# Optimization experiments

Hardware: AMD Instinct MI355X
Metric: run time of the kernel (lower is better)

## Reference

```python
import jax, jax.numpy as jnp
import numpy as np

B, L, C, N, D, FF, L2 = 1, 2400, 1536, 12, 128, 8960, 512
F_, H_, W_ = 2, 30, 40  # grid: L = F*H*W
EPS = 1e-6


def _rope_table(max_len=1024, d=D):
    # Wan rope_params: three bands of sizes d-4*(d//6), 2*(d//6), 2*(d//6)
    parts = [d - 4 * (d // 6), 2 * (d // 6), 2 * (d // 6)]
    pos = np.arange(max_len, dtype=np.float32)
    cs, ss = [], []
    for dp in parts:
        inv = 1.0 / (10000.0 ** (np.arange(0, dp, 2, dtype=np.float32) / dp))
        ang = np.outer(pos, inv)
        cs.append(np.cos(ang)); ss.append(np.sin(ang))
    return np.stack([np.concatenate(cs, 1), np.concatenate(ss, 1)], -1)  # [1024, d//2, 2]


def setup_inputs() -> dict:
    key = jax.random.key(0)
    ks = iter(jax.random.split(key, 48))
    def rn(shape, s=0.02):
        return jax.random.normal(next(ks), shape, dtype=jnp.float32) * s
    inp = dict(
        x=jax.random.normal(next(ks), (B, L, C), dtype=jnp.float32),
        e=rn((B, 1, 6, C), 0.5),
        context=jax.random.normal(next(ks), (B, L2, C), dtype=jnp.float32),
        freqs=jnp.asarray(_rope_table()),
        seq_lens=jnp.full((B,), L, dtype=jnp.int32),
        context_lens=jnp.full((B,), L2, dtype=jnp.int32),
        grid_sizes=jnp.array([[F_, H_, W_]], dtype=jnp.int32),
        modulation=rn((1, 6, C), 0.5),
    )
    for p in ('sa', 'ca'):
        for w in ('q', 'k', 'v', 'o'):
            inp[f'{p}_{w}_w'] = rn((C, C))
            inp[f'{p}_{w}_b'] = rn((C,))
        inp[f'{p}_nq_w'] = jnp.ones((C,), jnp.float32)
        inp[f'{p}_nk_w'] = jnp.ones((C,), jnp.float32)
    inp['ffn_w1'] = rn((C, FF)); inp['ffn_b1'] = rn((FF,))
    inp['ffn_w2'] = rn((FF, C)); inp['ffn_b2'] = rn((C,))
    return inp


def _rms_norm(x, w):
    v = jnp.mean(jnp.square(x), axis=-1, keepdims=True)
    return x * jax.lax.rsqrt(v + EPS) * w


def _layer_norm(x):
    m = jnp.mean(x, axis=-1, keepdims=True)
    v = jnp.mean(jnp.square(x - m), axis=-1, keepdims=True)
    return (x - m) * jax.lax.rsqrt(v + EPS)


def _apply_rope(x, freqs):
    # x: [B,S,N,D]; freqs: [1024, D//2, 2] (cos, sin). Wan default rope.
    c = D // 2
    p0, p1 = c - 2 * (c // 3), c // 3
    ft = jnp.broadcast_to(freqs[:F_, None, None, :p0], (F_, H_, W_, p0, 2))
    fh = jnp.broadcast_to(freqs[None, :H_, None, p0:p0 + p1], (F_, H_, W_, p1, 2))
    fw = jnp.broadcast_to(freqs[None, None, :W_, p0 + p1:], (F_, H_, W_, c - p0 - p1, 2))
    fr = jnp.concatenate([ft, fh, fw], axis=3).reshape(L, c, 2)
    cos = fr[..., 0][None, :, None, :]  # [1,S,1,c]
    sin = fr[..., 1][None, :, None, :]
    xp = x.reshape(B, x.shape[1], N, c, 2)  # interleaved (real, imag) pairs
    xr, xi = xp[..., 0], xp[..., 1]
    out = jnp.stack([xr * cos - xi * sin, xr * sin + xi * cos], axis=-1)
    return out.reshape(x.shape)


def _attention(q, k, v, k_len):
    # q:[B,Sq,N,D] k,v:[B,Sk,N,D]; dense softmax attention with k_lens mask
    scale = 1.0 / jnp.sqrt(jnp.float32(D))
    scores = jnp.einsum('bqnd,bknd->bnqk', q, k) * scale
    mask = jnp.arange(k.shape[1])[None, None, None, :] < k_len[:, None, None, None]
    scores = jnp.where(mask, scores, -jnp.inf)
    p = jax.nn.softmax(scores, axis=-1)
    return jnp.einsum('bnqk,bknd->bqnd', p, v)


def reference(x, e, context, freqs, seq_lens, context_lens, grid_sizes, modulation,
              sa_q_w, sa_q_b, sa_k_w, sa_k_b, sa_v_w, sa_v_b, sa_o_w, sa_o_b, sa_nq_w, sa_nk_w,
              ca_q_w, ca_q_b, ca_k_w, ca_k_b, ca_v_w, ca_v_b, ca_o_w, ca_o_b, ca_nq_w, ca_nk_w,
              ffn_w1, ffn_b1, ffn_w2, ffn_b2):
    # e: [B,1,6,C] (L1=1, broadcast over L == repeat_e); modulation: [1,6,C]
    em = modulation[None] + e  # [B,1,6,C]
    e0, e1, e2, e3, e4, e5 = (em[:, :, i] for i in range(6))  # each [B,1,C]
    # --- self attention with modulation ---
    h = e0 + _layer_norm(x) * (1.0 + e1)
    q = _rms_norm(h @ sa_q_w + sa_q_b, sa_nq_w).reshape(B, L, N, D)
    k = _rms_norm(h @ sa_k_w + sa_k_b, sa_nk_w).reshape(B, L, N, D)
    v = (h @ sa_v_w + sa_v_b).reshape(B, L, N, D)
    q = _apply_rope(q, freqs)
    k = _apply_rope(k, freqs)
    y = _attention(q, k, v, seq_lens).reshape(B, L, C)
    y = y @ sa_o_w + sa_o_b
    x = x + y * e2
    # --- cross attention (norm3 = Identity, cross_attn_norm=False) ---
    q = _rms_norm(x @ ca_q_w + ca_q_b, ca_nq_w).reshape(B, L, N, D)
    k = _rms_norm(context @ ca_k_w + ca_k_b, ca_nk_w).reshape(B, L2, N, D)
    v = (context @ ca_v_w + ca_v_b).reshape(B, L2, N, D)
    y = _attention(q, k, v, context_lens).reshape(B, L, C)
    x = x + (y @ ca_o_w + ca_o_b)
    # --- FFN with modulation ---
    h = e3 + _layer_norm(x) * (1.0 + e4)
    y = jax.nn.gelu(h @ ffn_w1 + ffn_b1, approximate=True) @ ffn_w2 + ffn_b2
    x = x + y * e5
    return x
```

## Files before the change

kernel.cpp:

```cpp
#include <hip/hip_runtime.h>
#include <cstddef>
#include <cstdint>

#define C_DIM   1536
#define L_SEQ   2400
#define L_CTX   512
#define N_HEADS 12
#define D_HEAD  128
#define FF_DIM  8960
#define F_GRID  2
#define H_GRID  30
#define W_GRID  40
#define EPS_F   1e-6f

#define ROPE_P0 22
#define ROPE_P1 43

typedef __attribute__((ext_vector_type(8))) short short8;
typedef __attribute__((ext_vector_type(4))) float f32x4;

__device__ inline unsigned short f2bf(float f) {
    union { float f; unsigned int u; } v; v.f = f;
    unsigned int r = v.u + 0x7FFF + ((v.u >> 16) & 1);
    return (unsigned short)(r >> 16);
}

#define GL2LDS(gp, lp) \
    __builtin_amdgcn_global_load_lds((const __attribute__((address_space(1))) void*)(gp), \
                                     (__attribute__((address_space(3))) void*)(lp), 16, 0, 0)

#define VMCNT6() asm volatile("s_waitcnt vmcnt(6)" ::: "memory")
#define VMCNT0() asm volatile("s_waitcnt vmcnt(0)" ::: "memory")
#define LGKM0()  asm volatile("s_waitcnt lgkmcnt(0)" ::: "memory")
#define BAR()    __builtin_amdgcn_s_barrier()


__global__ __launch_bounds__(256) void k_embed(const float* __restrict__ mod,
                                               const float* __restrict__ e,
                                               float* __restrict__ ev, int n) {
    int i = blockIdx.x * 256 + threadIdx.x;
    if (i < n) ev[i] = mod[i] + e[i];
}

__global__ __launch_bounds__(256) void k_catbias(float* __restrict__ dst,
                                                 const float* __restrict__ b0,
                                                 const float* __restrict__ b1,
                                                 const float* __restrict__ b2,
                                                 int ne, int n) {
    int i = blockIdx.x * 256 + threadIdx.x;
    if (i >= n) return;
    const float* s = (i < ne) ? b0 : (i < 2 * ne) ? b1 : b2;
    dst[i] = s[i % ne];
}

__global__ __launch_bounds__(256) void k_initbias(float* __restrict__ C,
                                                  const float* __restrict__ bias,
                                                  int n, int N) {
    int i4 = (blockIdx.x * 256 + threadIdx.x) * 4;
    if (i4 >= n) return;
    int col = i4 % N;
    *(float4*)(C + i4) = *(const float4*)(bias + col);
}

__global__ __launch_bounds__(256) void k_resid2(const float* __restrict__ a,
                                                const float* __restrict__ b,
                                                const float* __restrict__ ev, int ei,
                                                float* __restrict__ out,
                                                unsigned short* __restrict__ outb, int n) {
    int i = (blockIdx.x * 256 + threadIdx.x) * 2;
    if (i >= n) return;
    int c = i % C_DIM;
    float s0 = 1.f, s1 = 1.f;
    if (ei >= 0) {
        s0 = ev[ei * C_DIM + c];
        s1 = ev[ei * C_DIM + c + 1];
    }
    float2 av = *(const float2*)(a + i);
    float2 bv = *(const float2*)(b + i);
    float o0 = av.x + bv.x * s0;
    float o1 = av.y + bv.y * s1;
    *(float2*)(out + i) = make_float2(o0, o1);
    if (outb) {
        unsigned int pk = (unsigned int)f2bf(o0) | ((unsigned int)f2bf(o1) << 16);
        *(unsigned int*)(outb + i) = pk;
    }
}

__global__ __launch_bounds__(256) void k_tobf(const float* __restrict__ X,
                                              unsigned short* __restrict__ Y, int n) {
    int i = (blockIdx.x * 256 + threadIdx.x) * 2;
    if (i >= n) return;
    float2 v = *(const float2*)(X + i);
    unsigned int pk = (unsigned int)f2bf(v.x) | ((unsigned int)f2bf(v.y) << 16);
    *(unsigned int*)(Y + i) = pk;
}

__global__ __launch_bounds__(256) void k_lnmod_bf16(const float* __restrict__ X,
                                                    const float* __restrict__ ev,
                                                    int i0, int i1,
                                                    unsigned short* __restrict__ H) {
    __shared__ float rs[256];
    __shared__ float rs2[256];
    int row = blockIdx.x, tid = threadIdx.x;
    const float* xr = X + (size_t)row * C_DIM;
    float2 vals[3];
    float s = 0.f, s2 = 0.f;
#pragma unroll
    for (int i = 0; i < 3; ++i) {
        float2 v = *(const float2*)(xr + 2 * (tid + 256 * i));
        vals[i] = v;
        s += v.x + v.y; s2 += v.x * v.x + v.y * v.y;
    }
    rs[tid] = s; rs2[tid] = s2;
    __syncthreads();
    for (int st = 128; st > 0; st >>= 1) {
        if (tid < st) { rs[tid] += rs[tid + st]; rs2[tid] += rs2[tid + st]; }
        __syncthreads();
    }
    float mean = rs[0] * (1.0f / C_DIM);
    float var  = rs2[0] * (1.0f / C_DIM) - mean * mean;
    float rinv = rsqrtf(var + EPS_F);
    const float* E0 = ev + (size_t)i0 * C_DIM;
    const float* E1 = ev + (size_t)i1 * C_DIM;
    unsigned short* hr = H + (size_t)row * C_DIM;
#pragma unroll
    for (int i = 0; i < 3; ++i) {
        int c = 2 * (tid + 256 * i);
        float o0 = E0[c]     + (vals[i].x - mean) * rinv * (1.0f + E1[c]);
        float o1 = E0[c + 1] + (vals[i].y - mean) * rinv * (1.0f + E1[c + 1]);
        unsigned int pk = (unsigned int)f2bf(o0) | ((unsigned int)f2bf(o1) << 16);
        *(unsigned int*)(hr + c) = pk;
    }
}

__global__ __launch_bounds__(256) void k_rms_rope_bf16(const float* __restrict__ X,
                                                       const float* __restrict__ w,
                                                       const float* __restrict__ freqs,
                                                       int do_rope, float outscale,
                                                       unsigned short* __restrict__ Y,
                                                       int ldx) {
    __shared__ float rs[256];
    int row = blockIdx.x, tid = threadIdx.x;
    const float* xr = X + (size_t)row * ldx;
    float2 vals[3];
    float ss = 0.f;
#pragma unroll
    for (int i = 0; i < 3; ++i) {
        int p = tid + 256 * i;
        float2 v = *(const float2*)(xr + 2 * p);
        vals[i] = v;
        ss += v.x * v.x + v.y * v.y;
    }
    rs[tid] = ss;
    __syncthreads();
    for (int st = 128; st > 0; st >>= 1) {
        if (tid < st) rs[tid] += rs[tid + st];
        __syncthreads();
    }
    float rinv = rsqrtf(rs[0] * (1.0f / C_DIM) + EPS_F);
    int f = row / (H_GRID * W_GRID);
    int rem = row % (H_GRID * W_GRID);
    int hh = rem / W_GRID, ww = rem % W_GRID;
    unsigned short* yr = Y + (size_t)row * C_DIM;
#pragma unroll
    for (int i = 0; i < 3; ++i) {
        int p = tid + 256 * i;
        int c = 2 * p;
        float a = vals[i].x * rinv * w[c];
        float b = vals[i].y * rinv * w[c + 1];
        if (do_rope) {
            int j = p & 63;
            int idx = (j < ROPE_P0) ? f : (j < ROPE_P1) ? hh : ww;
            float cv = freqs[(idx * 64 + j) * 2 + 0];
            float sv = freqs[(idx * 64 + j) * 2 + 1];
            float na = a * cv - b * sv;
            float nb = a * sv + b * cv;
            a = na; b = nb;
        }
        a *= outscale; b *= outscale;
        unsigned int pk = (unsigned int)f2bf(a) | ((unsigned int)f2bf(b) << 16);
        *(unsigned int*)(yr + c) = pk;
    }
}

__global__ __launch_bounds__(256) void k_wt(const float* __restrict__ W,
                                            unsigned short* __restrict__ WT,
                                            int K, int N) {
    __shared__ float tile[32][33];
    int k0 = blockIdx.x * 32, n0 = blockIdx.y * 32;
    int t = threadIdx.x;
    int r = t >> 3, c4 = (t & 7) * 4;
    float4 v = *(const float4*)(W + (size_t)(k0 + r) * N + n0 + c4);
    tile[r][c4 + 0] = v.x; tile[r][c4 + 1] = v.y;
    tile[r][c4 + 2] = v.z; tile[r][c4 + 3] = v.w;
    __syncthreads();
    int n = t >> 3, k4 = (t & 7) * 4;
    uint2 o;
    o.x = (unsigned int)f2bf(tile[k4 + 0][n]) | ((unsigned int)f2bf(tile[k4 + 1][n]) << 16);
    o.y = (unsigned int)f2bf(tile[k4 + 2][n]) | ((unsigned int)f2bf(tile[k4 + 3][n]) << 16);
    *(uint2*)(WT + (size_t)(n0 + n) * K + k0 + k4) = o;
}

__global__ __launch_bounds__(256) void k_vt(const float* __restrict__ V,
                                            unsigned short* __restrict__ Vt, int Lk, int ldv) {
    __shared__ float tile[32][33];
    int k0 = blockIdx.x * 32, h = blockIdx.y, d0 = blockIdx.z * 32;
    int t = threadIdx.x;
    int k = t >> 3, d4 = (t & 7) * 4;
    float4 v = *(const float4*)(V + (size_t)(k0 + k) * ldv + h * D_HEAD + d0 + d4);
    tile[k][d4 + 0] = v.x; tile[k][d4 + 1] = v.y;
    tile[k][d4 + 2] = v.z; tile[k][d4 + 3] = v.w;
    __syncthreads();
    int d = t >> 3, k4 = (t & 7) * 4;
    uint2 o;
    o.x = (unsigned int)f2bf(tile[k4 + 0][d]) | ((unsigned int)f2bf(tile[k4 + 1][d]) << 16);
    o.y = (unsigned int)f2bf(tile[k4 + 2][d]) | ((unsigned int)f2bf(tile[k4 + 3][d]) << 16);
    *(uint2*)(Vt + (size_t)(h * D_HEAD + d0 + d) * Lk + k0 + k4) = o;
}

__global__ __launch_bounds__(256) void k_attn_mfma(const unsigned short* __restrict__ Qb,
                                                   const unsigned short* __restrict__ Kb,
                                                   const unsigned short* __restrict__ Vt,
                                                   unsigned short* __restrict__ O,
                                                   int Lq, int Lk) {
    __shared__ __align__(16) unsigned short Ks[32][136];
    __shared__ __align__(16) unsigned short Vs[128][40];
    __shared__ __align__(16) unsigned short Ps[4][16][40];
    const int tid = threadIdx.x;
    const int w = tid >> 6, lane = tid & 63;
    const int ln = lane & 15, lq = lane >> 4;
    const int h = blockIdx.y;
    const int q0 = blockIdx.x * 64 + w * 16;
    int qrow = q0 + ln; if (qrow >= Lq) qrow = Lq - 1;
    short8 qf[4];
#pragma unroll
    for (int c = 0; c < 4; ++c)
        qf[c] = *(const short8*)(Qb + (size_t)qrow * C_DIM + h * D_HEAD + c * 32 + lq * 8);
    f32x4 oacc[8];
#pragma unroll
    for (int t = 0; t < 8; ++t) oacc[t] = (f32x4){0.f, 0.f, 0.f, 0.f};
    float m_run[4] = {-3e38f, -3e38f, -3e38f, -3e38f};
    float l_run[4] = {0.f, 0.f, 0.f, 0.f};
    const float LOG2E = 1.4426950408889634f;

    for (int kb = 0; kb < Lk; kb += 32) {
        __syncthreads();
#pragma unroll
        for (int i = 0; i < 2; ++i) {
            int id = tid + i * 256;
            int r = id >> 4, c = id & 15;
            *(uint4*)&Ks[r][c * 8] =
                *(const uint4*)(Kb + (size_t)(kb + r) * C_DIM + h * D_HEAD + c * 8);
            int d = id >> 2, c2 = id & 3;
            *(uint4*)&Vs[d][c2 * 8] =
                *(const uint4*)(Vt + (size_t)(h * D_HEAD + d) * Lk + kb + c2 * 8);
        }
        __syncthreads();
        f32x4 c0 = (f32x4){0.f, 0.f, 0.f, 0.f};
        f32x4 c1 = (f32x4){0.f, 0.f, 0.f, 0.f};
#pragma unroll
        for (int c = 0; c < 4; ++c) {
            short8 b0 = *(const short8*)&Ks[ln][c * 32 + lq * 8];
            short8 b1 = *(const short8*)&Ks[16 + ln][c * 32 + lq * 8];
            c0 = __builtin_amdgcn_mfma_f32_16x16x32_bf16(qf[c], b0, c0, 0, 0, 0);
            c1 = __builtin_amdgcn_mfma_f32_16x16x32_bf16(qf[c], b1, c1, 0, 0, 0);
        }
        float alpha[4];
#pragma unroll
        for (int r = 0; r < 4; ++r) {
            float mx = fmaxf(c0[r], c1[r]);
            mx = fmaxf(mx, __shfl_xor(mx, 1));
            mx = fmaxf(mx, __shfl_xor(mx, 2));
            mx = fmaxf(mx, __shfl_xor(mx, 4));
            mx = fmaxf(mx, __shfl_xor(mx, 8));
            float mn = fmaxf(m_run[r], mx);
            alpha[r] = exp2f((m_run[r] - mn) * LOG2E);
            float p0 = exp2f((c0[r] - mn) * LOG2E);
            float p1 = exp2f((c1[r] - mn) * LOG2E);
            float s = p0 + p1;
            s += __shfl_xor(s, 1);
            s += __shfl_xor(s, 2);
            s += __shfl_xor(s, 4);
            s += __shfl_xor(s, 8);
            l_run[r] = l_run[r] * alpha[r] + s;
            m_run[r] = mn;
            Ps[w][lq * 4 + r][ln] = f2bf(p0);
            Ps[w][lq * 4 + r][16 + ln] = f2bf(p1);
        }
#pragma unroll
        for (int t = 0; t < 8; ++t)
#pragma unroll
            for (int r = 0; r < 4; ++r) oacc[t][r] *= alpha[r];
        short8 pa = *(const short8*)&Ps[w][ln][lq * 8];
#pragma unroll
        for (int t = 0; t < 8; ++t) {
            short8 bv = *(const short8*)&Vs[t * 16 + ln][lq * 8];
            oacc[t] = __builtin_amdgcn_mfma_f32_16x16x32_bf16(pa, bv, oacc[t], 0, 0, 0);
        }
    }
    float linv[4];
#pragma unroll
    for (int r = 0; r < 4; ++r) linv[r] = 1.0f / l_run[r];
#pragma unroll
    for (int t = 0; t < 8; ++t)
#pragma unroll
        for (int r = 0; r < 4; ++r) {
            int row = q0 + lq * 4 + r;
            if (row < Lq)
                O[(size_t)row * C_DIM + h * D_HEAD + t * 16 + ln] = f2bf(oacc[t][r] * linv[r]);
        }
}

__global__ __launch_bounds__(256) void k_gemm_bf16(const unsigned short* __restrict__ A,
                                                   const unsigned short* __restrict__ BT,
                                                   const float* __restrict__ bias,
                                                   float* __restrict__ Cf,
                                                   unsigned short* __restrict__ Cb,
                                                   int M, int N, int K, int Kc,
                                                   int gelu, int atomic) {
    __shared__ __align__(16) unsigned short As[128 * 32];
    __shared__ __align__(16) unsigned short Bs[128 * 32];
    const int tid = threadIdx.x;
    const int lane = tid & 63;
    const int w = tid >> 6;
    const int ln = lane & 15, lq = lane >> 4;
    const int wm = w >> 1, wn = w & 1;
    const int bm = blockIdx.y * 128, bn = blockIdx.x * 128;
    const int kb0 = blockIdx.z * Kc;

    int r0 = tid >> 2, c0 = (tid & 3) * 8;
    int ar0 = bm + r0;      if (ar0 >= M) ar0 = M - 1;
    int ar1 = bm + r0 + 64; if (ar1 >= M) ar1 = M - 1;
    const unsigned short* Ag0 = A + (size_t)ar0 * K + c0;
    const unsigned short* Ag1 = A + (size_t)ar1 * K + c0;
    const unsigned short* Bg0 = BT + (size_t)(bn + r0) * K + c0;
    const unsigned short* Bg1 = BT + (size_t)(bn + r0 + 64) * K + c0;
    unsigned short* Al0 = As + tid * 8;
    unsigned short* Al1 = As + 2048 + tid * 8;
    unsigned short* Bl0 = Bs + tid * 8;
    unsigned short* Bl1 = Bs + 2048 + tid * 8;

    f32x4 acc[4][4];
#pragma unroll
    for (int i = 0; i < 4; ++i)
#pragma unroll
        for (int j = 0; j < 4; ++j) acc[i][j] = (f32x4){0.f, 0.f, 0.f, 0.f};

    for (int kb = kb0; kb < kb0 + Kc; kb += 32) {
        __syncthreads();
        GL2LDS(Ag0 + kb, Al0);
        GL2LDS(Ag1 + kb, Al1);
        GL2LDS(Bg0 + kb, Bl0);
        GL2LDS(Bg1 + kb, Bl1);
        __syncthreads();
        short8 af[4], bf[4];
#pragma unroll
        for (int mi = 0; mi < 4; ++mi)
            af[mi] = *(const short8*)&As[(wm * 64 + mi * 16 + ln) * 32 + lq * 8];
#pragma unroll
        for (int ni = 0; ni < 4; ++ni)
            bf[ni] = *(const short8*)&Bs[(wn * 64 + ni * 16 + ln) * 32 + lq * 8];
#pragma unroll
        for (int mi = 0; mi < 4; ++mi)
#pragma unroll
            for (int ni = 0; ni < 4; ++ni)
                acc[mi][ni] = __builtin_amdgcn_mfma_f32_16x16x32_bf16(af[mi], bf[ni],
                                                                      acc[mi][ni], 0, 0, 0);
    }

#pragma unroll
    for (int ni = 0; ni < 4; ++ni) {
        int col = bn + wn * 64 + ni * 16 + ln;
        float bv = atomic ? 0.f : bias[col];
#pragma unroll
        for (int mi = 0; mi < 4; ++mi) {
#pragma unroll
            for (int r = 0; r < 4; ++r) {
                int row = bm + wm * 64 + mi * 16 + lq * 4 + r;
                if (row >= M) continue;
                if (atomic) {
                    atomicAdd(Cf + (size_t)row * N + col, acc[mi][ni][r]);
                } else if (gelu) {
                    float v = acc[mi][ni][r] + bv;
                    float u = 0.7978845608028654f * (v + 0.044715f * v * v * v);
                    float ex = __expf(2.f * u);
                    float t = 1.f - 2.f / (ex + 1.f);
                    Cb[(size_t)row * N + col] = f2bf(0.5f * v * (1.f + t));
                } else {
                    Cf[(size_t)row * N + col] = acc[mi][ni][r] + bv;
                }
            }
        }
    }
}

__global__ __launch_bounds__(512, 2) void k_gemm256(const unsigned short* __restrict__ A,
                                                    const unsigned short* __restrict__ BT,
                                                    const float* __restrict__ bias,
                                                    float* __restrict__ Cf,
                                                    unsigned short* __restrict__ Cb,
                                                    int M, int N, int K, int Kc,
                                                    int gelu, int atomic) {
    __shared__ __align__(16) unsigned short lds[2][2][2][128 * 64];
    const int tid = threadIdx.x;
    const int wid = tid >> 6, lane = tid & 63;
    const int ln = lane & 15, lq = lane >> 4;
    const int wm = wid >> 2, wn = wid & 3;
    const int bm = blockIdx.y * 256, bn = blockIdx.x * 256;
    const int kb0 = blockIdx.z * Kc;
    const int NT = Kc >> 6;
    const int NI = (NT + 1) >> 1;

    const int rr = tid >> 3;
    const int cc = (((tid & 7) ^ (rr & 7)) * 8);
    const unsigned short* aP[4];
    const unsigned short* bP[4];
#pragma unroll
    for (int g = 0; g < 4; ++g) {
        int ar = bm + g * 64 + rr; if (ar >= M) ar = M - 1;
        aP[g] = A + (size_t)ar * K + cc + kb0;
        bP[g] = BT + (size_t)(bn + g * 64 + rr) * K + cc + kb0;
    }

    f32x4 acc[8][4];
#pragma unroll
    for (int i = 0; i < 8; ++i)
#pragma unroll
        for (int j = 0; j < 4; ++j) acc[i][j] = (f32x4){0.f, 0.f, 0.f, 0.f};

    short8 af[4][2], bf0[2][2], bf1[2][2];

    const unsigned short* A0 = &lds[0][0][wm][0];
    const unsigned short* A1 = &lds[1][0][wm][0];
    const unsigned short* B0 = &lds[0][1][wn >> 1][0];
    const unsigned short* B1 = &lds[1][1][wn >> 1][0];

    auto stgA = [&](unsigned short* dst, int h, int kt) {
        GL2LDS(aP[h * 2 + 0] + (size_t)kt * 64, dst + tid * 8);
        GL2LDS(aP[h * 2 + 1] + (size_t)kt * 64, dst + 4096 + tid * 8);
    };
    auto stgB = [&](unsigned short* dst, int h, int kt) {
        GL2LDS(bP[h * 2 + 0] + (size_t)kt * 64, dst + tid * 8);
        GL2LDS(bP[h * 2 + 1] + (size_t)kt * 64, dst + 4096 + tid * 8);
    };
    auto rdA = [&](const unsigned short* Ab_, int mh) {
#pragma unroll
        for (int m4 = 0; m4 < 4; ++m4) {
            const int row = mh * 64 + m4 * 16 + ln;
#pragma unroll
            for (int ks = 0; ks < 2; ++ks) {
                const int sl = (ks * 4 + lq) ^ (ln & 7);
                af[m4][ks] = *(const short8*)&Ab_[row * 64 + sl * 8];
            }
        }
    };
    auto rdB = [&](const unsigned short* Bb_, int nh, short8 (&bfX)[2][2]) {
#pragma unroll
        for (int n2 = 0; n2 < 2; ++n2) {
            const int row = (wn & 1) * 64 + (nh * 2 + n2) * 16 + ln;
#pragma unroll
            for (int ks = 0; ks < 2; ++ks) {
                const int sl = (ks * 4 + lq) ^ (ln & 7);
                bfX[n2][ks] = *(const short8*)&Bb_[row * 64 + sl * 8];
            }
        }
    };
    auto mm = [&](int mh, int nh, short8 (&bfX)[2][2]) {
        __builtin_amdgcn_s_setprio(1);
#pragma unroll
        for (int m4 = 0; m4 < 4; ++m4)
#pragma unroll
            for (int n2 = 0; n2 < 2; ++n2)
#pragma unroll
                for (int ks = 0; ks < 2; ++ks)
                    acc[mh * 4 + m4][nh * 2 + n2] = __builtin_amdgcn_mfma_f32_16x16x32_bf16(
                        af[m4][ks], bfX[n2][ks], acc[mh * 4 + m4][nh * 2 + n2], 0, 0, 0);
        __builtin_amdgcn_s_setprio(0);
    };

    stgB(&lds[0][1][0][0], 0, 0); stgB(&lds[0][1][1][0], 1, 0);
    stgA(&lds[0][0][0][0], 0, 0);
    stgA(&lds[0][0][1][0], 1, 0);
    stgB(&lds[1][1][0][0], 0, 1);
    stgA(&lds[1][0][0][0], 0, 1); stgB(&lds[1][1][1][0], 1, 1);
    VMCNT6(); BAR();

    for (int k0 = 0; k0 < NI; ++k0) {
        const int a = 2 * k0, bT = a + 1;
        const bool last = (k0 == NI - 1);
        const bool hasB = (bT < NT);
        rdA(A0, 0); rdB(B0, 0, bf0);
        if (hasB) stgA(&lds[1][0][1][0], 1, bT);
        BAR(); LGKM0();
        mm(0, 0, bf0);
        BAR();
        rdB(B0, 1, bf1);
        BAR(); LGKM0();
        mm(0, 1, bf1);
        BAR();
        rdA(A0, 1);
        if (a + 2 < NT) { stgB(&lds[0][1][0][0], 0, a + 2); stgB(&lds[0][1][1][0], 1, a + 2); }
        BAR(); LGKM0();
        mm(1, 1, bf1);
        BAR();
        if (a + 2 < NT) stgA(&lds[0][0][0][0], 0, a + 2);
        BAR();
        mm(1, 0, bf0);
        if (!hasB) { BAR(); break; }
        if (last) { VMCNT0(); } else { VMCNT6(); }
        BAR();
        rdA(A1, 0); rdB(B1, 0, bf0);
        if (a + 2 < NT) stgA(&lds[0][0][1][0], 1, a + 2);
        BAR(); LGKM0();
        mm(0, 0, bf0);
        BAR();
        rdB(B1, 1, bf1);
        BAR(); LGKM0();
        mm(0, 1, bf1);
        BAR();
        rdA(A1, 1);
        if (bT + 2 < NT) stgB(&lds[1][1][0][0], 0, bT + 2);
        BAR(); LGKM0();
        mm(1, 1, bf1);
        BAR();
        if (bT + 2 < NT) { stgA(&lds[1][0][0][0], 0, bT + 2); stgB(&lds[1][1][1][0], 1, bT + 2); }
        BAR();
        mm(1, 0, bf0);
        if (k0 >= NI - 2) { VMCNT0(); } else { VMCNT6(); }
        BAR();
    }

#pragma unroll
    for (int ni = 0; ni < 4; ++ni) {
        int col = bn + wn * 64 + ni * 16 + ln;
        float bv = atomic ? 0.f : bias[col];
#pragma unroll
        for (int mi = 0; mi < 8; ++mi) {
#pragma unroll
            for (int r = 0; r < 4; ++r) {
                int row = bm + wm * 128 + mi * 16 + lq * 4 + r;
                if (row >= M) continue;
                if (atomic) {
                    atomicAdd(Cf + (size_t)row * N + col, acc[mi][ni][r]);
                } else if (gelu) {
                    float v = acc[mi][ni][r] + bv;
                    float u = 0.7978845608028654f * (v + 0.044715f * v * v * v);
                    float ex = __expf(2.f * u);
                    float t = 1.f - 2.f / (ex + 1.f);
                    Cb[(size_t)row * N + col] = f2bf(0.5f * v * (1.f + t));
                } else {
                    Cf[(size_t)row * N + col] = acc[mi][ni][r] + bv;
                }
            }
        }
    }
}

extern "C" void kernel_launch(void* const* d_in, const int* in_sizes, int n_in,
                              void* d_out, int out_size, void* d_ws, size_t ws_size,
                              hipStream_t stream) {
    const float* x          = (const float*)d_in[0];
    const float* e          = (const float*)d_in[1];
    const float* context    = (const float*)d_in[2];
    const float* freqs      = (const float*)d_in[3];
    const float* modulation = (const float*)d_in[7];
    const float* sa_q_w = (const float*)d_in[8];
    const float* sa_q_b = (const float*)d_in[9];
    const float* sa_k_w = (const float*)d_in[10];
    const float* sa_k_b = (const float*)d_in[11];
    const float* sa_v_w = (const float*)d_in[12];
    const float* sa_v_b = (const float*)d_in[13];
    const float* sa_o_w = (const float*)d_in[14];
    const float* sa_o_b = (const float*)d_in[15];
    const float* sa_nq  = (const float*)d_in[16];
    const float* sa_nk  = (const float*)d_in[17];
    const float* ca_q_w = (const float*)d_in[18];
    const float* ca_q_b = (const float*)d_in[19];
    const float* ca_k_w = (const float*)d_in[20];
    const float* ca_k_b = (const float*)d_in[21];
    const float* ca_v_w = (const float*)d_in[22];
    const float* ca_v_b = (const float*)d_in[23];
    const float* ca_o_w = (const float*)d_in[24];
    const float* ca_o_b = (const float*)d_in[25];
    const float* ca_nq  = (const float*)d_in[26];
    const float* ca_nk  = (const float*)d_in[27];
    const float* ffn_w1 = (const float*)d_in[28];
    const float* ffn_b1 = (const float*)d_in[29];
    const float* ffn_w2 = (const float*)d_in[30];
    const float* ffn_b2 = (const float*)d_in[31];

    const size_t LC = (size_t)L_SEQ * C_DIM;
    const size_t WMAX = (size_t)C_DIM * FF_DIM;
    char* p = (char*)d_ws;
    float* ev   = (float*)p;            p += 6 * C_DIM * sizeof(float);
    float* Bcat = (float*)p;            p += 3 * C_DIM * sizeof(float);
    float* Xcur = (float*)p;            p += LC * sizeof(float);
    float* Ebuf = (float*)p;            p += LC * sizeof(float);
    float* QKV  = (float*)p;            p += 3 * LC * sizeof(float);
    unsigned short* Ab = (unsigned short*)p;  p += LC * sizeof(short);
    unsigned short* Xb = (unsigned short*)p;  p += LC * sizeof(short);
    unsigned short* Qb = (unsigned short*)p;  p += LC * sizeof(short);
    unsigned short* Kb = (unsigned short*)p;  p += LC * sizeof(short);
    unsigned short* Vt = (unsigned short*)p;  p += LC * sizeof(short);
    unsigned short* Ob = (unsigned short*)p;  p += LC * sizeof(short);
    unsigned short* W0 = (unsigned short*)p;  p += WMAX * sizeof(short);
    unsigned short* W1 = (unsigned short*)p;  p += WMAX * sizeof(short);
    unsigned short* Fb = (unsigned short*)QKV;
    float* Pq    = QKV;
    float* ctxKV = QKV + LC;

    const int nLC = (int)LC;
    const float SCALE = 0.08838834764831845f;
    dim3 blk(256);
    dim3 blk512(512);
    dim3 g_qkv_256(4608 / 256, 10, 1);
    dim3 g_proj_s4(C_DIM / 128, 19, 4);
    dim3 g_ctxkv_s4(3072 / 128, L_CTX / 128, 4);
    dim3 g_ff1_256(FF_DIM / 256, 10, 1);
    dim3 g_ff2_256(C_DIM / 256, 10, 4);
    dim3 g_attn((L_SEQ + 63) / 64, N_HEADS);
    dim3 g_vt_s(L_SEQ / 32, N_HEADS, 4);
    dim3 g_vt_c(L_CTX / 32, N_HEADS, 4);
    dim3 g_wt_cc(C_DIM / 32, C_DIM / 32);
    dim3 g_wt_w1(C_DIM / 32, FF_DIM / 32);
    dim3 g_wt_w2(FF_DIM / 32, C_DIM / 32);
    dim3 g_half(nLC / 512);
    dim3 g_init_cc(nLC / 1024);
    dim3 g_init_kv(L_CTX * 3072 / 1024);

    k_embed<<<dim3((6 * C_DIM + 255) / 256), blk, 0, stream>>>(modulation, e, ev, 6 * C_DIM);

    k_catbias<<<dim3((3 * C_DIM + 255) / 256), blk, 0, stream>>>(Bcat, sa_q_b, sa_k_b, sa_v_b,
                                                                 C_DIM, 3 * C_DIM);
    k_wt<<<g_wt_cc, blk, 0, stream>>>(sa_q_w, W0, C_DIM, C_DIM);
    k_wt<<<g_wt_cc, blk, 0, stream>>>(sa_k_w, W0 + (size_t)C_DIM * C_DIM, C_DIM, C_DIM);
    k_wt<<<g_wt_cc, blk, 0, stream>>>(sa_v_w, W0 + (size_t)2 * C_DIM * C_DIM, C_DIM, C_DIM);
    k_lnmod_bf16<<<dim3(L_SEQ), blk, 0, stream>>>(x, ev, 0, 1, Ab);
    k_gemm256<<<g_qkv_256, blk512, 0, stream>>>(Ab, W0, Bcat, QKV, nullptr,
                                                L_SEQ, 4608, C_DIM, C_DIM, 0, 0);
    k_wt<<<g_wt_cc, blk, 0, stream>>>(sa_o_w, W1, C_DIM, C_DIM);
    k_rms_rope_bf16<<<dim3(L_SEQ), blk, 0, stream>>>(QKV, sa_nq, freqs, 1, SCALE, Qb, 4608);
    k_rms_rope_bf16<<<dim3(L_SEQ), blk, 0, stream>>>(QKV + C_DIM, sa_nk, freqs, 1, 1.0f, Kb, 4608);
    k_vt<<<g_vt_s, blk, 0, stream>>>(QKV + 2 * C_DIM, Vt, L_SEQ, 4608);
    k_attn_mfma<<<g_attn, blk, 0, stream>>>(Qb, Kb, Vt, Ob, L_SEQ, L_SEQ);
    k_initbias<<<g_init_cc, blk, 0, stream>>>(Ebuf, sa_o_b, nLC, C_DIM);
    k_gemm_bf16<<<g_proj_s4, blk, 0, stream>>>(Ob, W1, nullptr, Ebuf, nullptr,
                                               L_SEQ, C_DIM, C_DIM, 384, 0, 1);
    k_resid2<<<g_half, blk, 0, stream>>>(x, Ebuf, ev, 2, Xcur, Xb, nLC);

    k_wt<<<g_wt_cc, blk, 0, stream>>>(ca_q_w, W0, C_DIM, C_DIM);
    k_wt<<<g_wt_cc, blk, 0, stream>>>(ca_k_w, W1, C_DIM, C_DIM);
    k_wt<<<g_wt_cc, blk, 0, stream>>>(ca_v_w, W1 + (size_t)C_DIM * C_DIM, C_DIM, C_DIM);
    k_tobf<<<dim3(L_CTX * C_DIM / 512), blk, 0, stream>>>(context, Ab, L_CTX * C_DIM);
    k_catbias<<<dim3((2 * C_DIM + 255) / 256), blk, 0, stream>>>(Bcat, ca_k_b, ca_v_b, nullptr,
                                                                 C_DIM, 2 * C_DIM);
    k_initbias<<<g_init_cc, blk, 0, stream>>>(Pq, ca_q_b, nLC, C_DIM);
    k_gemm_bf16<<<g_proj_s4, blk, 0, stream>>>(Xb, W0, nullptr, Pq, nullptr,
                                               L_SEQ, C_DIM, C_DIM, 384, 0, 1);
    k_initbias<<<g_init_kv, blk, 0, stream>>>(ctxKV, Bcat, L_CTX * 3072, 3072);
    k_gemm_bf16<<<g_ctxkv_s4, blk, 0, stream>>>(Ab, W1, nullptr, ctxKV, nullptr,
                                                L_CTX, 3072, C_DIM, 384, 0, 1);
    k_rms_rope_bf16<<<dim3(L_SEQ), blk, 0, stream>>>(Pq, ca_nq, freqs, 0, SCALE, Qb, C_DIM);
    k_rms_rope_bf16<<<dim3(L_CTX), blk, 0, stream>>>(ctxKV, ca_nk, freqs, 0, 1.0f, Kb, 3072);
    k_vt<<<g_vt_c, blk, 0, stream>>>(ctxKV + C_DIM, Vt, L_CTX, 3072);
    k_attn_mfma<<<g_attn, blk, 0, stream>>>(Qb, Kb, Vt, Ob, L_SEQ, L_CTX);
    k_wt<<<g_wt_cc, blk, 0, stream>>>(ca_o_w, W0, C_DIM, C_DIM);
    k_initbias<<<g_init_cc, blk, 0, stream>>>(Ebuf, ca_o_b, nLC, C_DIM);
    k_gemm_bf16<<<g_proj_s4, blk, 0, stream>>>(Ob, W0, nullptr, Ebuf, nullptr,
                                               L_SEQ, C_DIM, C_DIM, 384, 0, 1);
    k_resid2<<<g_half, blk, 0, stream>>>(Xcur, Ebuf, (const float*)nullptr, -1, Xcur, nullptr, nLC);

    k_wt<<<g_wt_w1, blk, 0, stream>>>(ffn_w1, W1, C_DIM, FF_DIM);
    k_lnmod_bf16<<<dim3(L_SEQ), blk, 0, stream>>>(Xcur, ev, 3, 4, Ab);
    k_gemm256<<<g_ff1_256, blk512, 0, stream>>>(Ab, W1, ffn_b1, nullptr, Fb,
                                                L_SEQ, FF_DIM, C_DIM, C_DIM, 1, 0);
    k_wt<<<g_wt_w2, blk, 0, stream>>>(ffn_w2, W0, FF_DIM, C_DIM);
    k_initbias<<<g_init_cc, blk, 0, stream>>>(Ebuf, ffn_b2, nLC, C_DIM);
    k_gemm256<<<g_ff2_256, blk512, 0, stream>>>(Fb, W0, nullptr, Ebuf, nullptr,
                                                L_SEQ, C_DIM, FF_DIM, 2240, 0, 1);
    k_resid2<<<g_half, blk, 0, stream>>>(Xcur, Ebuf, ev, 5, (float*)d_out, nullptr, nLC);
}
```

Before: 1.098 ms.

## Widen attention key tiles with swizzled async loads and lazy rescale; route projections to 256-tile GEMM

The attention kernel now processes 64 keys per iteration instead of 32. K and V tiles are loaded straight into XOR-swizzled shared memory with global-to-LDS copies, which avoids bank conflicts and register staging. It also skips the rescale of the output accumulator unless the running max grows by more than a threshold (lazy rescaling). Separately, the 128-tile projection GEMM is removed and all projection and context K/V GEMMs use the 256-tile kernel with split-K. This cuts barriers and per-tile overhead in attention, but the threshold-based rescale could cause overflow issues and edge handling for partial tiles grows more complex.

Measured after the change: 1.042 ms. 5.1% less time.

```diff
diff --git a/kernel.cpp b/kernel.cpp
--- a/kernel.cpp
+++ b/kernel.cpp
@@ -223,9 +223,9 @@
                                                    const unsigned short* __restrict__ Vt,
                                                    unsigned short* __restrict__ O,
                                                    int Lq, int Lk) {
-    __shared__ __align__(16) unsigned short Ks[32][136];
-    __shared__ __align__(16) unsigned short Vs[128][40];
-    __shared__ __align__(16) unsigned short Ps[4][16][40];
+    __shared__ __align__(16) unsigned short Ks[64 * 128];
+    __shared__ __align__(16) unsigned short Vs[128 * 64];
+    __shared__ __align__(16) unsigned short Ps[4][16][68];
     const int tid = threadIdx.x;
     const int w = tid >> 6, lane = tid & 63;
     const int ln = lane & 15, lq = lane >> 4;
@@ -236,66 +236,113 @@
 #pragma unroll
     for (int c = 0; c < 4; ++c)
         qf[c] = *(const short8*)(Qb + (size_t)qrow * C_DIM + h * D_HEAD + c * 32 + lq * 8);
+
+    const int r0k = tid >> 4, sk = tid & 15;
+    const int kxor = r0k & 7;
+    const int kcol = h * D_HEAD + (sk ^ kxor) * 8;
+    int rowK[4];
+    unsigned short* dK[4];
+#pragma unroll
+    for (int j = 0; j < 4; ++j) {
+        rowK[j] = r0k + 16 * j;
+        dK[j] = (unsigned short*)Ks + ((size_t)tid + 256 * j) * 8;
+    }
+    const int d0v = tid >> 3, sv = tid & 7;
+    const int vxor = d0v & 7;
+    const int vslot = (sv ^ vxor) * 8;
+    int dRow[4];
+    unsigned short* dV[4];
+#pragma unroll
+    for (int j = 0; j < 4; ++j) {
+        dRow[j] = h * D_HEAD + d0v + 32 * j;
+        dV[j] = (unsigned short*)Vs + ((size_t)tid + 256 * j) * 8;
+    }
+
     f32x4 oacc[8];
 #pragma unroll
     for (int t = 0; t < 8; ++t) oacc[t] = (f32x4){0.f, 0.f, 0.f, 0.f};
     float m_run[4] = {-3e38f, -3e38f, -3e38f, -3e38f};
     float l_run[4] = {0.f, 0.f, 0.f, 0.f};
     const float LOG2E = 1.4426950408889634f;
-
-    for (int kb = 0; kb < Lk; kb += 32) {
+    const int lx = ln & 7;
+
+    for (int kb = 0; kb < Lk; kb += 64) {
+        const bool gv2 = (kb + 32) < Lk;
         __syncthreads();
 #pragma unroll
-        for (int i = 0; i < 2; ++i) {
-            int id = tid + i * 256;
-            int r = id >> 4, c = id & 15;
-            *(uint4*)&Ks[r][c * 8] =
-                *(const uint4*)(Kb + (size_t)(kb + r) * C_DIM + h * D_HEAD + c * 8);
-            int d = id >> 2, c2 = id & 3;
-            *(uint4*)&Vs[d][c2 * 8] =
-                *(const uint4*)(Vt + (size_t)(h * D_HEAD + d) * Lk + kb + c2 * 8);
+        for (int j = 0; j < 4; ++j) {
+            int kr = kb + rowK[j]; if (kr >= Lk) kr = Lk - 1;
+            GL2LDS(Kb + (size_t)kr * C_DIM + kcol, dK[j]);
+            int vc = kb + vslot; if (vc + 8 > Lk) vc = Lk - 8;
+            GL2LDS(Vt + (size_t)dRow[j] * Lk + vc, dV[j]);
         }
         __syncthreads();
-        f32x4 c0 = (f32x4){0.f, 0.f, 0.f, 0.f};
-        f32x4 c1 = (f32x4){0.f, 0.f, 0.f, 0.f};
+
+        f32x4 c0 = (f32x4){0.f,0.f,0.f,0.f}, c1 = c0, c2 = c0, c3 = c0;
 #pragma unroll
         for (int c = 0; c < 4; ++c) {
-            short8 b0 = *(const short8*)&Ks[ln][c * 32 + lq * 8];
-            short8 b1 = *(const short8*)&Ks[16 + ln][c * 32 + lq * 8];
+            const int slt = ((c * 4 + lq) ^ lx) * 8;
+            short8 b0 = *(const short8*)&Ks[(size_t)(ln) * 128 + slt];
+            short8 b1 = *(const short8*)&Ks[(size_t)(16 + ln) * 128 + slt];
             c0 = __builtin_amdgcn_mfma_f32_16x16x32_bf16(qf[c], b0, c0, 0, 0, 0);
             c1 = __builtin_amdgcn_mfma_f32_16x16x32_bf16(qf[c], b1, c1, 0, 0, 0);
-        }
-        float alpha[4];
+            if (gv2) {
+                short8 b2 = *(const short8*)&Ks[(size_t)(32 + ln) * 128 + slt];
+                short8 b3 = *(const short8*)&Ks[(size_t)(48 + ln) * 128 + slt];
+                c2 = __builtin_amdgcn_mfma_f32_16x16x32_bf16(qf[c], b2, c2, 0, 0, 0);
+                c3 = __builtin_amdgcn_mfma_f32_16x16x32_bf16(qf[c], b3, c3, 0, 0, 0);
+            }
+        }
+
 #pragma unroll
         for (int r = 0; r < 4; ++r) {
             float mx = fmaxf(c0[r], c1[r]);
+            if (gv2) mx = fmaxf(mx, fmaxf(c2[r], c3[r]));
             mx = fmaxf(mx, __shfl_xor(mx, 1));
             mx = fmaxf(mx, __shfl_xor(mx, 2));
             mx = fmaxf(mx, __shfl_xor(mx, 4));
             mx = fmaxf(mx, __shfl_xor(mx, 8));
-            float mn = fmaxf(m_run[r], mx);
-            alpha[r] = exp2f((m_run[r] - mn) * LOG2E);
+            float mn = m_run[r];
+            float a = 1.f;
+            if (__any(mx > mn + 8.f)) {
+                float m2 = fmaxf(mn, mx);
+                a = exp2f((mn - m2) * LOG2E);
+                mn = m2;
+                m_run[r] = m2;
+#pragma unroll
+                for (int t = 0; t < 8; ++t) oacc[t][r] *= a;
+            }
             float p0 = exp2f((c0[r] - mn) * LOG2E);
             float p1 = exp2f((c1[r] - mn) * LOG2E);
-            float s = p0 + p1;
+            float p2 = gv2 ? exp2f((c2[r] - mn) * LOG2E) : 0.f;
+            float p3 = gv2 ? exp2f((c3[r] - mn) * LOG2E) : 0.f;
+            float s = p0 + p1 + p2 + p3;
             s += __shfl_xor(s, 1);
             s += __shfl_xor(s, 2);
             s += __shfl_xor(s, 4);
             s += __shfl_xor(s, 8);
-            l_run[r] = l_run[r] * alpha[r] + s;
-            m_run[r] = mn;
+            l_run[r] = l_run[r] * a + s;
             Ps[w][lq * 4 + r][ln] = f2bf(p0);
             Ps[w][lq * 4 + r][16 + ln] = f2bf(p1);
-        }
-#pragma unroll
-        for (int t = 0; t < 8; ++t)
-#pragma unroll
-            for (int r = 0; r < 4; ++r) oacc[t][r] *= alpha[r];
-        short8 pa = *(const short8*)&Ps[w][ln][lq * 8];
+            if (gv2) {
+                Ps[w][lq * 4 + r][32 + ln] = f2bf(p2);
+                Ps[w][lq * 4 + r][48 + ln] = f2bf(p3);
+            }
+        }
+
+        short8 pa0 = *(const short8*)&Ps[w][ln][lq * 8];
 #pragma unroll
         for (int t = 0; t < 8; ++t) {
-            short8 bv = *(const short8*)&Vs[t * 16 + ln][lq * 8];
-            oacc[t] = __builtin_amdgcn_mfma_f32_16x16x32_bf16(pa, bv, oacc[t], 0, 0, 0);
+            short8 bv = *(const short8*)&Vs[(size_t)(t * 16 + ln) * 64 + ((lq ^ lx) * 8)];
+            oacc[t] = __builtin_amdgcn_mfma_f32_16x16x32_bf16(pa0, bv, oacc[t], 0, 0, 0);
+        }
+        if (gv2) {
+            short8 pa1 = *(const short8*)&Ps[w][ln][32 + lq * 8];
+#pragma unroll
+            for (int t = 0; t < 8; ++t) {
+                short8 bv = *(const short8*)&Vs[(size_t)(t * 16 + ln) * 64 + (((4 + lq) ^ lx) * 8)];
+                oacc[t] = __builtin_amdgcn_mfma_f32_16x16x32_bf16(pa1, bv, oacc[t], 0, 0, 0);
+            }
         }
     }
     float linv[4];
@@ -309,89 +356,6 @@
             if (row < Lq)
                 O[(size_t)row * C_DIM + h * D_HEAD + t * 16 + ln] = f2bf(oacc[t][r] * linv[r]);
         }
-}
-
-__global__ __launch_bounds__(256) void k_gemm_bf16(const unsigned short* __restrict__ A,
-                                                   const unsigned short* __restrict__ BT,
-                                                   const float* __restrict__ bias,
-                                                   float* __restrict__ Cf,
-                                                   unsigned short* __restrict__ Cb,
-                                                   int M, int N, int K, int Kc,
-                                                   int gelu, int atomic) {
-    __shared__ __align__(16) unsigned short As[128 * 32];
-    __shared__ __align__(16) unsigned short Bs[128 * 32];
-    const int tid = threadIdx.x;
-    const int lane = tid & 63;
-    const int w = tid >> 6;
-    const int ln = lane & 15, lq = lane >> 4;
-    const int wm = w >> 1, wn = w & 1;
-    const int bm = blockIdx.y * 128, bn = blockIdx.x * 128;
-    const int kb0 = blockIdx.z * Kc;
-
-    int r0 = tid >> 2, c0 = (tid & 3) * 8;
-    int ar0 = bm + r0;      if (ar0 >= M) ar0 = M - 1;
-    int ar1 = bm + r0 + 64; if (ar1 >= M) ar1 = M - 1;
-    const unsigned short* Ag0 = A + (size_t)ar0 * K + c0;
-    const unsigned short* Ag1 = A + (size_t)ar1 * K + c0;
-    const unsigned short* Bg0 = BT + (size_t)(bn + r0) * K + c0;
-    const unsigned short* Bg1 = BT + (size_t)(bn + r0 + 64) * K + c0;
-    unsigned short* Al0 = As + tid * 8;
-    unsigned short* Al1 = As + 2048 + tid * 8;
-    unsigned short* Bl0 = Bs + tid * 8;
-    unsigned short* Bl1 = Bs + 2048 + tid * 8;
-
-    f32x4 acc[4][4];
-#pragma unroll
-    for (int i = 0; i < 4; ++i)
-#pragma unroll
-        for (int j = 0; j < 4; ++j) acc[i][j] = (f32x4){0.f, 0.f, 0.f, 0.f};
-
-    for (int kb = kb0; kb < kb0 + Kc; kb += 32) {
-        __syncthreads();
-        GL2LDS(Ag0 + kb, Al0);
-        GL2LDS(Ag1 + kb, Al1);
-        GL2LDS(Bg0 + kb, Bl0);
-        GL2LDS(Bg1 + kb, Bl1);
-        __syncthreads();
-        short8 af[4], bf[4];
-#pragma unroll
-        for (int mi = 0; mi < 4; ++mi)
-            af[mi] = *(const short8*)&As[(wm * 64 + mi * 16 + ln) * 32 + lq * 8];
-#pragma unroll
-        for (int ni = 0; ni < 4; ++ni)
-            bf[ni] = *(const short8*)&Bs[(wn * 64 + ni * 16 + ln) * 32 + lq * 8];
-#pragma unroll
-        for (int mi = 0; mi < 4; ++mi)
-#pragma unroll
-            for (int ni = 0; ni < 4; ++ni)
-                acc[mi][ni] = __builtin_amdgcn_mfma_f32_16x16x32_bf16(af[mi], bf[ni],
-                                                                      acc[mi][ni], 0, 0, 0);
-    }
-
-#pragma unroll
-    for (int ni = 0; ni < 4; ++ni) {
-        int col = bn + wn * 64 + ni * 16 + ln;
-        float bv = atomic ? 0.f : bias[col];
-#pragma unroll
-        for (int mi = 0; mi < 4; ++mi) {
-#pragma unroll
-            for (int r = 0; r < 4; ++r) {
-                int row = bm + wm * 64 + mi * 16 + lq * 4 + r;
-                if (row >= M) continue;
-                if (atomic) {
-                    atomicAdd(Cf + (size_t)row * N + col, acc[mi][ni][r]);
-                } else if (gelu) {
-                    float v = acc[mi][ni][r] + bv;
-                    float u = 0.7978845608028654f * (v + 0.044715f * v * v * v);
-                    float ex = __expf(2.f * u);
-                    float t = 1.f - 2.f / (ex + 1.f);
-                    Cb[(size_t)row * N + col] = f2bf(0.5f * v * (1.f + t));
-                } else {
-                    Cf[(size_t)row * N + col] = acc[mi][ni][r] + bv;
-                }
-            }
-        }
-    }
 }
 
 __global__ __launch_bounds__(512, 2) void k_gemm256(const unsigned short* __restrict__ A,
@@ -614,8 +578,8 @@
     dim3 blk(256);
     dim3 blk512(512);
     dim3 g_qkv_256(4608 / 256, 10, 1);
-    dim3 g_proj_s4(C_DIM / 128, 19, 4);
-    dim3 g_ctxkv_s4(3072 / 128, L_CTX / 128, 4);
+    dim3 g_proj_256(C_DIM / 256, 10, 4);
+    dim3 g_ctxkv_256(3072 / 256, L_CTX / 256, 4);
     dim3 g_ff1_256(FF_DIM / 256, 10, 1);
     dim3 g_ff2_256(C_DIM / 256, 10, 4);
     dim3 g_attn((L_SEQ + 63) / 64, N_HEADS);
@@ -644,8 +608,8 @@
     k_vt<<<g_vt_s, blk, 0, stream>>>(QKV + 2 * C_DIM, Vt, L_SEQ, 4608);
     k_attn_mfma<<<g_attn, blk, 0, stream>>>(Qb, Kb, Vt, Ob, L_SEQ, L_SEQ);
     k_initbias<<<g_init_cc, blk, 0, stream>>>(Ebuf, sa_o_b, nLC, C_DIM);
-    k_gemm_bf16<<<g_proj_s4, blk, 0, stream>>>(Ob, W1, nullptr, Ebuf, nullptr,
-                                               L_SEQ, C_DIM, C_DIM, 384, 0, 1);
+    k_gemm256<<<g_proj_256, blk512, 0, stream>>>(Ob, W1, nullptr, Ebuf, nullptr,
+                                                 L_SEQ, C_DIM, C_DIM, 384, 0, 1);
     k_resid2<<<g_half, blk, 0, stream>>>(x, Ebuf, ev, 2, Xcur, Xb, nLC);
 
     k_wt<<<g_wt_cc, blk, 0, stream>>>(ca_q_w, W0, C_DIM, C_DIM);
@@ -655,19 +619,19 @@
     k_catbias<<<dim3((2 * C_DIM + 255) / 256), blk, 0, stream>>>(Bcat, ca_k_b, ca_v_b, nullptr,
                                                                  C_DIM, 2 * C_DIM);
     k_initbias<<<g_init_cc, blk, 0, stream>>>(Pq, ca_q_b, nLC, C_DIM);
-    k_gemm_bf16<<<g_proj_s4, blk, 0, stream>>>(Xb, W0, nullptr, Pq, nullptr,
-                                               L_SEQ, C_DIM, C_DIM, 384, 0, 1);
+    k_gemm256<<<g_proj_256, blk512, 0, stream>>>(Xb, W0, nullptr, Pq, nullptr,
+                                                 L_SEQ, C_DIM, C_DIM, 384, 0, 1);
     k_initbias<<<g_init_kv, blk, 0, stream>>>(ctxKV, Bcat, L_CTX * 3072, 3072);
-    k_gemm_bf16<<<g_ctxkv_s4, blk, 0, stream>>>(Ab, W1, nullptr, ctxKV, nullptr,
-                                                L_CTX, 3072, C_DIM, 384, 0, 1);
+    k_gemm256<<<g_ctxkv_256, blk512, 0, stream>>>(Ab, W1, nullptr, ctxKV, nullptr,
+                                                  L_CTX, 3072, C_DIM, 384, 0, 1);
     k_rms_rope_bf16<<<dim3(L_SEQ), blk, 0, stream>>>(Pq, ca_nq, freqs, 0, SCALE, Qb, C_DIM);
     k_rms_rope_bf16<<<dim3(L_CTX), blk, 0, stream>>>(ctxKV, ca_nk, freqs, 0, 1.0f, Kb, 3072);
     k_vt<<<g_vt_c, blk, 0, stream>>>(ctxKV + C_DIM, Vt, L_CTX, 3072);
     k_attn_mfma<<<g_attn, blk, 0, stream>>>(Qb, Kb, Vt, Ob, L_SEQ, L_CTX);
     k_wt<<<g_wt_cc, blk, 0, stream>>>(ca_o_w, W0, C_DIM, C_DIM);
     k_initbias<<<g_init_cc, blk, 0, stream>>>(Ebuf, ca_o_b, nLC, C_DIM);
-    k_gemm_bf16<<<g_proj_s4, blk, 0, stream>>>(Ob, W0, nullptr, Ebuf, nullptr,
-                                               L_SEQ, C_DIM, C_DIM, 384, 0, 1);
+    k_gemm256<<<g_proj_256, blk512, 0, stream>>>(Ob, W0, nullptr, Ebuf, nullptr,
+                                                 L_SEQ, C_DIM, C_DIM, 384, 0, 1);
     k_resid2<<<g_half, blk, 0, stream>>>(Xcur, Ebuf, (const float*)nullptr, -1, Xcur, nullptr, nLC);
 
     k_wt<<<g_wt_w1, blk, 0, stream>>>(ffn_w1, W1, C_DIM, FF_DIM);
```
